# Performance work log

Measured on AMD Instinct MI355X. Metric: run time of the kernel, lower is better.

## Reference

```python
import jax, jax.numpy as jnp
import numpy as np

HIDDEN = 768
META = 25
ED_COUNT = 300
B, N_MENT, N_PAIRS = 2, 2000, 40000


def setup_inputs() -> dict:
    key = jax.random.key(0)
    ks = jax.random.split(key, 8)
    mention_reprs = jax.random.normal(ks[0], (B, N_MENT, HIDDEN), dtype=jnp.float32)
    coref_mention_pairs = jax.random.randint(ks[1], (B, N_PAIRS, 2), 0, N_MENT)
    coref_eds = jax.random.randint(ks[2], (B, N_PAIRS), 0, ED_COUNT)
    in_dim = HIDDEN * 2 + META
    # nn.Linear default init scale ~ 1/sqrt(fan_in); exact init is irrelevant for correctness
    W1 = jax.random.normal(ks[3], (in_dim, HIDDEN), dtype=jnp.float32) / np.sqrt(in_dim)
    b1 = jnp.zeros((HIDDEN,), dtype=jnp.float32)
    W2 = jax.random.normal(ks[4], (HIDDEN, 1), dtype=jnp.float32) / np.sqrt(HIDDEN)
    b2 = jnp.zeros((1,), dtype=jnp.float32)
    ed_table = jax.random.normal(ks[5], (ED_COUNT, META), dtype=jnp.float32)
    return {
        "mention_reprs": mention_reprs,
        "coref_mention_pairs": coref_mention_pairs,
        "coref_eds": coref_eds,
        "ed_table": ed_table,
        "W1": W1,
        "b1": b1,
        "W2": W2,
        "b2": b2,
    }


def reference(mention_reprs, coref_mention_pairs, coref_eds, ed_table, W1, b1, W2, b2):
    b = mention_reprs.shape[0]
    # batch_index gather: [B, P, 2, H]
    bidx = jnp.arange(b)[:, None, None]
    pairs = mention_reprs[bidx, coref_mention_pairs]
    # flatten pair dim -> [B, P, 2H]
    pair_repr = pairs.reshape(b, pairs.shape[1], -1)
    eds = ed_table[coref_eds]  # [B, P, META]
    coref_repr = jnp.concatenate([pair_repr, eds], axis=2)  # [B, P, 2H+META]
    h = jax.nn.relu(coref_repr @ W1 + b1)  # dropout = identity in eval
    logits = (h @ W2 + b2).squeeze(-1)  # [B, P]
    return logits
```

## Files before the change

### kernel.cpp

```cpp
#include <hip/hip_runtime.h>
#include <stdint.h>

#define HIDDEN 768
#define META 25
#define EDC 300
#define BB 2
#define NMENT 2000
#define NPAIRS 40000
#define M_ROWS (BB * NMENT)
#define M_PAD 4096
#define N_OUT 1536
#define TOTAL_PAIRS (BB * NPAIRS)
#define BK 64

typedef __bf16 bf16x8 __attribute__((ext_vector_type(8)));
typedef float f32x4 __attribute__((ext_vector_type(4)));

static __device__ __forceinline__ float bf2f(unsigned short u) {
    union { unsigned int u; float f; } v; v.u = ((unsigned int)u) << 16; return v.f;
}
static __device__ __forceinline__ float2 bf2x(unsigned int u) {
    union { unsigned int x; float f; } lo, hi;
    lo.x = u << 16; hi.x = u & 0xffff0000u;
    float2 r; r.x = lo.f; r.y = hi.f; return r;
}
static __device__ __forceinline__ unsigned short f2bf(float f) {
    union { float f; unsigned int u; } v; v.f = f;
    unsigned int u = v.u;
    unsigned int r = (u + 0x7FFFu + ((u >> 16) & 1u)) >> 16;
    return (unsigned short)r;
}

#define GLOAD_LDS16(g, l)                                                            \
    __builtin_amdgcn_global_load_lds((const __attribute__((address_space(1))) void*)(g), \
                                     (__attribute__((address_space(3))) void*)(l), 16, 0, 0)

#define NB_CONVM 3072
#define NB_CONVW 576
#define NB_PREP  900
#define NB_W2    3

__global__ __launch_bounds__(256) void k_prep_all(
        const float* __restrict__ M, unsigned short* __restrict__ Mb,
        const float* __restrict__ W1, unsigned short* __restrict__ Wt,
        const float* __restrict__ ed_table, const float* __restrict__ b1,
        unsigned short* __restrict__ Epp,
        const float* __restrict__ W2, unsigned short* __restrict__ W2b) {
    const int blk = blockIdx.x;
    const int t = threadIdx.x;
    if (blk < NB_CONVM) {
        int idx = (blk * 256 + t) * 4;
        int row = idx / HIDDEN;
        ushort4 o;
        if (row < M_ROWS) {
            const float4 v = *(const float4*)(M + idx);
            o.x = f2bf(v.x); o.y = f2bf(v.y); o.z = f2bf(v.z); o.w = f2bf(v.w);
        } else {
            o.x = 0; o.y = 0; o.z = 0; o.w = 0;
        }
        *(ushort4*)(Mb + idx) = o;
    } else if (blk < NB_CONVM + NB_CONVW) {
        __shared__ float tile[32][68];
        int id = blk - NB_CONVM;
        int nt = id % 24, kt = id / 24;
        int n0 = nt * 64, k0 = kt * 32;
        int tk = t >> 4, tn = (t & 15) * 4;
        int srcRowOff = (n0 < HIDDEN) ? 0 : HIDDEN;
        int srcColBase = (n0 < HIDDEN) ? n0 : (n0 - HIDDEN);
        {
            const float4 v0 = *(const float4*)(W1 + (size_t)(k0 + tk + srcRowOff) * HIDDEN + srcColBase + tn);
            tile[tk][tn] = v0.x; tile[tk][tn + 1] = v0.y; tile[tk][tn + 2] = v0.z; tile[tk][tn + 3] = v0.w;
            const float4 v1 = *(const float4*)(W1 + (size_t)(k0 + tk + 16 + srcRowOff) * HIDDEN + srcColBase + tn);
            tile[tk + 16][tn] = v1.x; tile[tk + 16][tn + 1] = v1.y; tile[tk + 16][tn + 2] = v1.z; tile[tk + 16][tn + 3] = v1.w;
        }
        __syncthreads();
        int wn = t >> 2, wk = (t & 3) * 8;
        unsigned int p0 = (unsigned int)f2bf(tile[wk + 0][wn]) | ((unsigned int)f2bf(tile[wk + 1][wn]) << 16);
        unsigned int p1 = (unsigned int)f2bf(tile[wk + 2][wn]) | ((unsigned int)f2bf(tile[wk + 3][wn]) << 16);
        unsigned int p2 = (unsigned int)f2bf(tile[wk + 4][wn]) | ((unsigned int)f2bf(tile[wk + 5][wn]) << 16);
        unsigned int p3 = (unsigned int)f2bf(tile[wk + 6][wn]) | ((unsigned int)f2bf(tile[wk + 7][wn]) << 16);
        uint4 pk; pk.x = p0; pk.y = p1; pk.z = p2; pk.w = p3;
        *(uint4*)(Wt + (size_t)(n0 + wn) * HIDDEN + k0 + wk) = pk;
    } else if (blk < NB_CONVM + NB_CONVW + NB_PREP) {
        int id = (blk - NB_CONVM - NB_CONVW) * 256 + t;
        int e = id / HIDDEN, n = id - e * HIDDEN;
        float acc = b1[n];
#pragma unroll
        for (int k = 0; k < META; k++)
            acc += ed_table[e * META + k] * W1[(size_t)(2 * HIDDEN + k) * HIDDEN + n];
        Epp[id] = f2bf(acc);
    } else {
        int id = (blk - NB_CONVM - NB_CONVW - NB_PREP) * 256 + t;
        if (id < HIDDEN) W2b[id] = f2bf(W2[id]);
    }
}

__global__ __launch_bounds__(256) void k_gemm(const unsigned short* __restrict__ Mb,
                                              const unsigned short* __restrict__ Wt,
                                              unsigned short* __restrict__ AW) {
    __shared__ unsigned short As[128 * BK];
    __shared__ unsigned short Bs[64 * BK];
    const int m0 = blockIdx.x * 128;
    const int n0 = blockIdx.y * 64;
    const int t = threadIdx.x, w = t >> 6, lane = t & 63;
    const int wm = (w & 1) * 64, wn = (w >> 1) * 32;
    const int q = lane >> 4, r = lane & 15;
    const int lrow = lane >> 3;
    const int lcol = ((((lane & 7) - lrow) & 7)) * 8;
    const unsigned short* gA = Mb + (size_t)(m0 + w * 32 + lrow) * HIDDEN + lcol;
    const unsigned short* gB = Wt + (size_t)(n0 + w * 16 + lrow) * HIDDEN + lcol;
    unsigned short* lA = As + (w * 32) * BK;
    unsigned short* lB = Bs + (w * 16) * BK;
    f32x4 acc[4][2] = {};
    for (int k0 = 0; k0 < HIDDEN; k0 += BK) {
        GLOAD_LDS16(gA + k0, lA);
        GLOAD_LDS16(gA + k0 + 8 * HIDDEN,  lA + 8 * BK);
        GLOAD_LDS16(gA + k0 + 16 * HIDDEN, lA + 16 * BK);
        GLOAD_LDS16(gA + k0 + 24 * HIDDEN, lA + 24 * BK);
        GLOAD_LDS16(gB + k0, lB);
        GLOAD_LDS16(gB + k0 + 8 * HIDDEN,  lB + 8 * BK);
        __syncthreads();
        bf16x8 af[4][2], bfr[2][2];
        const int rs = r & 7;
#pragma unroll
        for (int i = 0; i < 4; i++)
#pragma unroll
            for (int s = 0; s < 2; s++)
                af[i][s] = *(const bf16x8*)&As[(wm + i * 16 + r) * BK + 8 * ((q + 4 * s + rs) & 7)];
#pragma unroll
        for (int j = 0; j < 2; j++)
#pragma unroll
            for (int s = 0; s < 2; s++)
                bfr[j][s] = *(const bf16x8*)&Bs[(wn + j * 16 + r) * BK + 8 * ((q + 4 * s + rs) & 7)];
#pragma unroll
        for (int i = 0; i < 4; i++)
#pragma unroll
            for (int j = 0; j < 2; j++) {
                acc[i][j] = __builtin_amdgcn_mfma_f32_16x16x32_bf16(af[i][0], bfr[j][0], acc[i][j], 0, 0, 0);
                acc[i][j] = __builtin_amdgcn_mfma_f32_16x16x32_bf16(af[i][1], bfr[j][1], acc[i][j], 0, 0, 0);
            }
        __syncthreads();
    }
    const int colb = n0 + wn + (lane & 15);
    const int rowb = m0 + wm + (lane >> 4) * 4;
#pragma unroll
    for (int i = 0; i < 4; i++)
#pragma unroll
        for (int j = 0; j < 2; j++) {
            unsigned short* dst = AW + (size_t)(rowb + i * 16) * N_OUT + colb + j * 16;
#pragma unroll
            for (int reg = 0; reg < 4; reg++)
                dst[(size_t)reg * N_OUT] = f2bf(acc[i][j][reg]);
        }
}

__global__ __launch_bounds__(256) void k_pair(const unsigned short* __restrict__ AW,
                                              const unsigned short* __restrict__ Epp,
                                              const unsigned short* __restrict__ W2b,
                                              const float* __restrict__ b2,
                                              const int* __restrict__ pairs,
                                              const int* __restrict__ eds,
                                              float* __restrict__ out) {
    const int wid = blockIdx.x * 4 + (threadIdx.x >> 6);
    const int lane = threadIdx.x & 63;
    const int p0 = wid * 4;
    const int b = (p0 >= NPAIRS) ? 1 : 0;
    const int n0 = lane * 8;
    const int n1 = 512 + (lane & 31) * 8;
    const bool lo = lane < 32;

    const int4 pr01 = *(const int4*)(pairs + (size_t)p0 * 2);
    const int4 pr23 = *(const int4*)(pairs + (size_t)p0 * 2 + 4);
    const int4 ed4  = *(const int4*)(eds + p0);

    const size_t base = (size_t)(b * NMENT);
    const unsigned short* a1p0 = AW + (base + pr01.x) * N_OUT;
    const unsigned short* a2p0 = AW + (base + pr01.y) * N_OUT + HIDDEN;
    const unsigned short* ep0  = Epp + (size_t)ed4.x * HIDDEN;
    const unsigned short* a1p1 = AW + (base + pr01.z) * N_OUT;
    const unsigned short* a2p1 = AW + (base + pr01.w) * N_OUT + HIDDEN;
    const unsigned short* ep1  = Epp + (size_t)ed4.y * HIDDEN;
    const unsigned short* a1p2 = AW + (base + pr23.x) * N_OUT;
    const unsigned short* a2p2 = AW + (base + pr23.y) * N_OUT + HIDDEN;
    const unsigned short* ep2  = Epp + (size_t)ed4.z * HIDDEN;
    const unsigned short* a1p3 = AW + (base + pr23.z) * N_OUT;
    const unsigned short* a2p3 = AW + (base + pr23.w) * N_OUT + HIDDEN;
    const unsigned short* ep3  = Epp + (size_t)ed4.w * HIDDEN;

    const unsigned short* c01a = lo ? a1p0 : a1p1;
    const unsigned short* c01b = lo ? a2p0 : a2p1;
    const unsigned short* c01e = lo ? ep0  : ep1;
    const unsigned short* c23a = lo ? a1p2 : a1p3;
    const unsigned short* c23b = lo ? a2p2 : a2p3;
    const unsigned short* c23e = lo ? ep2  : ep3;

    uint4 w0 = *(const uint4*)(W2b + n0);
    uint4 wc = *(const uint4*)(W2b + n1);
    uint4 x1 = *(const uint4*)(a1p0 + n0), x2 = *(const uint4*)(a2p0 + n0), xe = *(const uint4*)(ep0 + n0);
    uint4 y1 = *(const uint4*)(a1p1 + n0), y2 = *(const uint4*)(a2p1 + n0), ye = *(const uint4*)(ep1 + n0);
    uint4 z1 = *(const uint4*)(a1p2 + n0), z2 = *(const uint4*)(a2p2 + n0), ze = *(const uint4*)(ep2 + n0);
    uint4 v1 = *(const uint4*)(a1p3 + n0), v2 = *(const uint4*)(a2p3 + n0), ve = *(const uint4*)(ep3 + n0);
    uint4 q1 = *(const uint4*)(c01a + n1), q2 = *(const uint4*)(c01b + n1), qe = *(const uint4*)(c01e + n1);
    uint4 s1 = *(const uint4*)(c23a + n1), s2 = *(const uint4*)(c23b + n1), se = *(const uint4*)(c23e + n1);

    float acc0 = 0.f, acc1 = 0.f, acc2 = 0.f, acc3 = 0.f;
    float cacc01 = 0.f, cacc23 = 0.f;
#define ACC2(acc, ua, ub, ue, uw)                                              \
    {                                                                          \
        float2 fa = bf2x(ua), fb = bf2x(ub), fe = bf2x(ue), fw = bf2x(uw);     \
        float h0 = fmaxf(fa.x + fb.x + fe.x, 0.f);                             \
        float h1 = fmaxf(fa.y + fb.y + fe.y, 0.f);                             \
        acc += h0 * fw.x + h1 * fw.y;                                          \
    }
    ACC2(acc0, x1.x, x2.x, xe.x, w0.x); ACC2(acc0, x1.y, x2.y, xe.y, w0.y);
    ACC2(acc0, x1.z, x2.z, xe.z, w0.z); ACC2(acc0, x1.w, x2.w, xe.w, w0.w);
    ACC2(acc1, y1.x, y2.x, ye.x, w0.x); ACC2(acc1, y1.y, y2.y, ye.y, w0.y);
    ACC2(acc1, y1.z, y2.z, ye.z, w0.z); ACC2(acc1, y1.w, y2.w, ye.w, w0.w);
    ACC2(acc2, z1.x, z2.x, ze.x, w0.x); ACC2(acc2, z1.y, z2.y, ze.y, w0.y);
    ACC2(acc2, z1.z, z2.z, ze.z, w0.z); ACC2(acc2, z1.w, z2.w, ze.w, w0.w);
    ACC2(acc3, v1.x, v2.x, ve.x, w0.x); ACC2(acc3, v1.y, v2.y, ve.y, w0.y);
    ACC2(acc3, v1.z, v2.z, ve.z, w0.z); ACC2(acc3, v1.w, v2.w, ve.w, w0.w);
    ACC2(cacc01, q1.x, q2.x, qe.x, wc.x); ACC2(cacc01, q1.y, q2.y, qe.y, wc.y);
    ACC2(cacc01, q1.z, q2.z, qe.z, wc.z); ACC2(cacc01, q1.w, q2.w, qe.w, wc.w);
    ACC2(cacc23, s1.x, s2.x, se.x, wc.x); ACC2(cacc23, s1.y, s2.y, se.y, wc.y);
    ACC2(cacc23, s1.z, s2.z, se.z, wc.z); ACC2(cacc23, s1.w, s2.w, se.w, wc.w);
#undef ACC2
#pragma unroll
    for (int o = 32; o > 0; o >>= 1) {
        acc0 += __shfl_xor(acc0, o, 64);
        acc1 += __shfl_xor(acc1, o, 64);
        acc2 += __shfl_xor(acc2, o, 64);
        acc3 += __shfl_xor(acc3, o, 64);
    }
#pragma unroll
    for (int o = 16; o > 0; o >>= 1) {
        cacc01 += __shfl_xor(cacc01, o, 64);
        cacc23 += __shfl_xor(cacc23, o, 64);
    }
    const float t0 = __shfl(cacc01, 0, 64);
    const float t1 = __shfl(cacc01, 32, 64);
    const float t2 = __shfl(cacc23, 0, 64);
    const float t3 = __shfl(cacc23, 32, 64);
    if (lane == 0) {
        float bias = b2[0];
        float4 o;
        o.x = acc0 + t0 + bias;
        o.y = acc1 + t1 + bias;
        o.z = acc2 + t2 + bias;
        o.w = acc3 + t3 + bias;
        *(float4*)(out + p0) = o;
    }
}

extern "C" void kernel_launch(void* const* d_in, const int* in_sizes, int n_in,
                              void* d_out, int out_size, void* d_ws, size_t ws_size,
                              hipStream_t stream) {
    const float* mention  = (const float*)d_in[0];
    const int*   pairs    = (const int*)d_in[1];
    const int*   eds      = (const int*)d_in[2];
    const float* ed_table = (const float*)d_in[3];
    const float* W1       = (const float*)d_in[4];
    const float* b1       = (const float*)d_in[5];
    const float* W2       = (const float*)d_in[6];
    const float* b2       = (const float*)d_in[7];
    float* out = (float*)d_out;

    char* ws = (char*)d_ws;
    unsigned short* Mb  = (unsigned short*)(ws);
    unsigned short* Wt  = (unsigned short*)(ws + 6291456);
    unsigned short* AW  = (unsigned short*)(ws + 8650752);
    unsigned short* Epp = (unsigned short*)(ws + 21233664);
    unsigned short* W2b = (unsigned short*)(ws + 21694464);

    k_prep_all<<<dim3(NB_CONVM + NB_CONVW + NB_PREP + NB_W2), dim3(256), 0, stream>>>(
        mention, Mb, W1, Wt, ed_table, b1, Epp, W2, W2b);
    k_gemm<<<dim3(M_PAD / 128, N_OUT / 64), dim3(256), 0, stream>>>(Mb, Wt, AW);
    k_pair<<<dim3(TOTAL_PAIRS / 16), dim3(256), 0, stream>>>(AW, Epp, W2b, b2, pairs, eds, out);
}
```

Measured before the change: 115.8 us.

## Fuse prep, GEMM and pair kernels into one cooperative persistent kernel

Merges the three launches (conversion/prep, bf16 GEMM, pair gather-reduce) into a single cooperative kernel. Blocks loop over the former grid indices, and grid-wide syncs separate the phases. The aim is to remove launch overhead and inter-kernel gaps. In exchange it adds grid barrier costs and caps the grid at resident occupancy (at most 768 blocks), which can reduce latency hiding in the memory-bound pair phase.

```diff
diff --git a/kernel.cpp b/kernel.cpp
--- a/kernel.cpp
+++ b/kernel.cpp
@@ -1,5 +1,8 @@
 #include <hip/hip_runtime.h>
+#include <hip/hip_cooperative_groups.h>
 #include <stdint.h>
+
+namespace cg = cooperative_groups;
 
 #define HIDDEN 768
 #define META 25
@@ -16,9 +19,6 @@
 typedef __bf16 bf16x8 __attribute__((ext_vector_type(8)));
 typedef float f32x4 __attribute__((ext_vector_type(4)));
 
-static __device__ __forceinline__ float bf2f(unsigned short u) {
-    union { unsigned int u; float f; } v; v.u = ((unsigned int)u) << 16; return v.f;
-}
 static __device__ __forceinline__ float2 bf2x(unsigned int u) {
     union { unsigned int x; float f; } lo, hi;
     lo.x = u << 16; hi.x = u & 0xffff0000u;
@@ -39,172 +39,180 @@
 #define NB_CONVW 576
 #define NB_PREP  900
 #define NB_W2    3
-
-__global__ __launch_bounds__(256) void k_prep_all(
+#define NB_TOT   (NB_CONVM + NB_CONVW + NB_PREP + NB_W2)
+#define NB_GEMM  768
+#define NB_PAIR  (TOTAL_PAIRS / 16)
+
+__global__ __launch_bounds__(256, 3) void k_fused(
         const float* __restrict__ M, unsigned short* __restrict__ Mb,
         const float* __restrict__ W1, unsigned short* __restrict__ Wt,
         const float* __restrict__ ed_table, const float* __restrict__ b1,
         unsigned short* __restrict__ Epp,
-        const float* __restrict__ W2, unsigned short* __restrict__ W2b) {
-    const int blk = blockIdx.x;
-    const int t = threadIdx.x;
-    if (blk < NB_CONVM) {
-        int idx = (blk * 256 + t) * 4;
-        int row = idx / HIDDEN;
-        ushort4 o;
-        if (row < M_ROWS) {
-            const float4 v = *(const float4*)(M + idx);
-            o.x = f2bf(v.x); o.y = f2bf(v.y); o.z = f2bf(v.z); o.w = f2bf(v.w);
-        } else {
-            o.x = 0; o.y = 0; o.z = 0; o.w = 0;
-        }
-        *(ushort4*)(Mb + idx) = o;
-    } else if (blk < NB_CONVM + NB_CONVW) {
-        __shared__ float tile[32][68];
-        int id = blk - NB_CONVM;
-        int nt = id % 24, kt = id / 24;
-        int n0 = nt * 64, k0 = kt * 32;
-        int tk = t >> 4, tn = (t & 15) * 4;
-        int srcRowOff = (n0 < HIDDEN) ? 0 : HIDDEN;
-        int srcColBase = (n0 < HIDDEN) ? n0 : (n0 - HIDDEN);
-        {
-            const float4 v0 = *(const float4*)(W1 + (size_t)(k0 + tk + srcRowOff) * HIDDEN + srcColBase + tn);
-            tile[tk][tn] = v0.x; tile[tk][tn + 1] = v0.y; tile[tk][tn + 2] = v0.z; tile[tk][tn + 3] = v0.w;
-            const float4 v1 = *(const float4*)(W1 + (size_t)(k0 + tk + 16 + srcRowOff) * HIDDEN + srcColBase + tn);
-            tile[tk + 16][tn] = v1.x; tile[tk + 16][tn + 1] = v1.y; tile[tk + 16][tn + 2] = v1.z; tile[tk + 16][tn + 3] = v1.w;
-        }
-        __syncthreads();
-        int wn = t >> 2, wk = (t & 3) * 8;
-        unsigned int p0 = (unsigned int)f2bf(tile[wk + 0][wn]) | ((unsigned int)f2bf(tile[wk + 1][wn]) << 16);
-        unsigned int p1 = (unsigned int)f2bf(tile[wk + 2][wn]) | ((unsigned int)f2bf(tile[wk + 3][wn]) << 16);
-        unsigned int p2 = (unsigned int)f2bf(tile[wk + 4][wn]) | ((unsigned int)f2bf(tile[wk + 5][wn]) << 16);
-        unsigned int p3 = (unsigned int)f2bf(tile[wk + 6][wn]) | ((unsigned int)f2bf(tile[wk + 7][wn]) << 16);
-        uint4 pk; pk.x = p0; pk.y = p1; pk.z = p2; pk.w = p3;
-        *(uint4*)(Wt + (size_t)(n0 + wn) * HIDDEN + k0 + wk) = pk;
-    } else if (blk < NB_CONVM + NB_CONVW + NB_PREP) {
-        int id = (blk - NB_CONVM - NB_CONVW) * 256 + t;
-        int e = id / HIDDEN, n = id - e * HIDDEN;
-        float acc = b1[n];
-#pragma unroll
-        for (int k = 0; k < META; k++)
-            acc += ed_table[e * META + k] * W1[(size_t)(2 * HIDDEN + k) * HIDDEN + n];
-        Epp[id] = f2bf(acc);
-    } else {
-        int id = (blk - NB_CONVM - NB_CONVW - NB_PREP) * 256 + t;
-        if (id < HIDDEN) W2b[id] = f2bf(W2[id]);
-    }
-}
-
-__global__ __launch_bounds__(256) void k_gemm(const unsigned short* __restrict__ Mb,
-                                              const unsigned short* __restrict__ Wt,
-                                              unsigned short* __restrict__ AW) {
+        const float* __restrict__ W2, unsigned short* __restrict__ W2b,
+        const float* __restrict__ b2,
+        const int* __restrict__ pairs, const int* __restrict__ eds,
+        unsigned short* __restrict__ AW, float* __restrict__ out) {
     __shared__ unsigned short As[128 * BK];
     __shared__ unsigned short Bs[64 * BK];
-    const int m0 = blockIdx.x * 128;
-    const int n0 = blockIdx.y * 64;
-    const int t = threadIdx.x, w = t >> 6, lane = t & 63;
-    const int wm = (w & 1) * 64, wn = (w >> 1) * 32;
-    const int q = lane >> 4, r = lane & 15;
-    const int lrow = lane >> 3;
-    const int lcol = ((((lane & 7) - lrow) & 7)) * 8;
-    const unsigned short* gA = Mb + (size_t)(m0 + w * 32 + lrow) * HIDDEN + lcol;
-    const unsigned short* gB = Wt + (size_t)(n0 + w * 16 + lrow) * HIDDEN + lcol;
-    unsigned short* lA = As + (w * 32) * BK;
-    unsigned short* lB = Bs + (w * 16) * BK;
-    f32x4 acc[4][2] = {};
-    for (int k0 = 0; k0 < HIDDEN; k0 += BK) {
-        GLOAD_LDS16(gA + k0, lA);
-        GLOAD_LDS16(gA + k0 + 8 * HIDDEN,  lA + 8 * BK);
-        GLOAD_LDS16(gA + k0 + 16 * HIDDEN, lA + 16 * BK);
-        GLOAD_LDS16(gA + k0 + 24 * HIDDEN, lA + 24 * BK);
-        GLOAD_LDS16(gB + k0, lB);
-        GLOAD_LDS16(gB + k0 + 8 * HIDDEN,  lB + 8 * BK);
-        __syncthreads();
-        bf16x8 af[4][2], bfr[2][2];
-        const int rs = r & 7;
-#pragma unroll
-        for (int i = 0; i < 4; i++)
-#pragma unroll
-            for (int s = 0; s < 2; s++)
-                af[i][s] = *(const bf16x8*)&As[(wm + i * 16 + r) * BK + 8 * ((q + 4 * s + rs) & 7)];
-#pragma unroll
-        for (int j = 0; j < 2; j++)
-#pragma unroll
-            for (int s = 0; s < 2; s++)
-                bfr[j][s] = *(const bf16x8*)&Bs[(wn + j * 16 + r) * BK + 8 * ((q + 4 * s + rs) & 7)];
-#pragma unroll
-        for (int i = 0; i < 4; i++)
-#pragma unroll
-            for (int j = 0; j < 2; j++) {
-                acc[i][j] = __builtin_amdgcn_mfma_f32_16x16x32_bf16(af[i][0], bfr[j][0], acc[i][j], 0, 0, 0);
-                acc[i][j] = __builtin_amdgcn_mfma_f32_16x16x32_bf16(af[i][1], bfr[j][1], acc[i][j], 0, 0, 0);
-            }
-        __syncthreads();
-    }
-    const int colb = n0 + wn + (lane & 15);
-    const int rowb = m0 + wm + (lane >> 4) * 4;
-#pragma unroll
-    for (int i = 0; i < 4; i++)
-#pragma unroll
-        for (int j = 0; j < 2; j++) {
-            unsigned short* dst = AW + (size_t)(rowb + i * 16) * N_OUT + colb + j * 16;
-#pragma unroll
-            for (int reg = 0; reg < 4; reg++)
-                dst[(size_t)reg * N_OUT] = f2bf(acc[i][j][reg]);
+    __shared__ float tile[32][68];
+    const int t = threadIdx.x;
+    const int NG = gridDim.x;
+
+    for (int blk = blockIdx.x; blk < NB_TOT; blk += NG) {
+        if (blk < NB_CONVM) {
+            int idx = (blk * 256 + t) * 4;
+            int row = idx / HIDDEN;
+            ushort4 o;
+            if (row < M_ROWS) {
+                const float4 v = *(const float4*)(M + idx);
+                o.x = f2bf(v.x); o.y = f2bf(v.y); o.z = f2bf(v.z); o.w = f2bf(v.w);
+            } else {
+                o.x = 0; o.y = 0; o.z = 0; o.w = 0;
+            }
+            *(ushort4*)(Mb + idx) = o;
+        } else if (blk < NB_CONVM + NB_CONVW) {
+            int id = blk - NB_CONVM;
+            int nt = id % 24, kt = id / 24;
+            int n0 = nt * 64, k0 = kt * 32;
+            int tk = t >> 4, tn = (t & 15) * 4;
+            int srcRowOff = (n0 < HIDDEN) ? 0 : HIDDEN;
+            int srcColBase = (n0 < HIDDEN) ? n0 : (n0 - HIDDEN);
+            {
+                const float4 v0 = *(const float4*)(W1 + (size_t)(k0 + tk + srcRowOff) * HIDDEN + srcColBase + tn);
+                tile[tk][tn] = v0.x; tile[tk][tn + 1] = v0.y; tile[tk][tn + 2] = v0.z; tile[tk][tn + 3] = v0.w;
+                const float4 v1 = *(const float4*)(W1 + (size_t)(k0 + tk + 16 + srcRowOff) * HIDDEN + srcColBase + tn);
+                tile[tk + 16][tn] = v1.x; tile[tk + 16][tn + 1] = v1.y; tile[tk + 16][tn + 2] = v1.z; tile[tk + 16][tn + 3] = v1.w;
+            }
+            __syncthreads();
+            int wn = t >> 2, wk = (t & 3) * 8;
+            unsigned int p0 = (unsigned int)f2bf(tile[wk + 0][wn]) | ((unsigned int)f2bf(tile[wk + 1][wn]) << 16);
+            unsigned int p1 = (unsigned int)f2bf(tile[wk + 2][wn]) | ((unsigned int)f2bf(tile[wk + 3][wn]) << 16);
+            unsigned int p2 = (unsigned int)f2bf(tile[wk + 4][wn]) | ((unsigned int)f2bf(tile[wk + 5][wn]) << 16);
+            unsigned int p3 = (unsigned int)f2bf(tile[wk + 6][wn]) | ((unsigned int)f2bf(tile[wk + 7][wn]) << 16);
+            uint4 pk; pk.x = p0; pk.y = p1; pk.z = p2; pk.w = p3;
+            *(uint4*)(Wt + (size_t)(n0 + wn) * HIDDEN + k0 + wk) = pk;
+            __syncthreads();
+        } else if (blk < NB_CONVM + NB_CONVW + NB_PREP) {
+            int id = (blk - NB_CONVM - NB_CONVW) * 256 + t;
+            int e = id / HIDDEN, n = id - e * HIDDEN;
+            float acc = b1[n];
+#pragma unroll
+            for (int k = 0; k < META; k++)
+                acc += ed_table[e * META + k] * W1[(size_t)(2 * HIDDEN + k) * HIDDEN + n];
+            Epp[id] = f2bf(acc);
+        } else {
+            int id = (blk - NB_CONVM - NB_CONVW - NB_PREP) * 256 + t;
+            if (id < HIDDEN) W2b[id] = f2bf(W2[id]);
         }
-}
-
-__global__ __launch_bounds__(256) void k_pair(const unsigned short* __restrict__ AW,
-                                              const unsigned short* __restrict__ Epp,
-                                              const unsigned short* __restrict__ W2b,
-                                              const float* __restrict__ b2,
-                                              const int* __restrict__ pairs,
-                                              const int* __restrict__ eds,
-                                              float* __restrict__ out) {
-    const int wid = blockIdx.x * 4 + (threadIdx.x >> 6);
-    const int lane = threadIdx.x & 63;
-    const int p0 = wid * 4;
-    const int b = (p0 >= NPAIRS) ? 1 : 0;
-    const int n0 = lane * 8;
-    const int n1 = 512 + (lane & 31) * 8;
-    const bool lo = lane < 32;
-
-    const int4 pr01 = *(const int4*)(pairs + (size_t)p0 * 2);
-    const int4 pr23 = *(const int4*)(pairs + (size_t)p0 * 2 + 4);
-    const int4 ed4  = *(const int4*)(eds + p0);
-
-    const size_t base = (size_t)(b * NMENT);
-    const unsigned short* a1p0 = AW + (base + pr01.x) * N_OUT;
-    const unsigned short* a2p0 = AW + (base + pr01.y) * N_OUT + HIDDEN;
-    const unsigned short* ep0  = Epp + (size_t)ed4.x * HIDDEN;
-    const unsigned short* a1p1 = AW + (base + pr01.z) * N_OUT;
-    const unsigned short* a2p1 = AW + (base + pr01.w) * N_OUT + HIDDEN;
-    const unsigned short* ep1  = Epp + (size_t)ed4.y * HIDDEN;
-    const unsigned short* a1p2 = AW + (base + pr23.x) * N_OUT;
-    const unsigned short* a2p2 = AW + (base + pr23.y) * N_OUT + HIDDEN;
-    const unsigned short* ep2  = Epp + (size_t)ed4.z * HIDDEN;
-    const unsigned short* a1p3 = AW + (base + pr23.z) * N_OUT;
-    const unsigned short* a2p3 = AW + (base + pr23.w) * N_OUT + HIDDEN;
-    const unsigned short* ep3  = Epp + (size_t)ed4.w * HIDDEN;
-
-    const unsigned short* c01a = lo ? a1p0 : a1p1;
-    const unsigned short* c01b = lo ? a2p0 : a2p1;
-    const unsigned short* c01e = lo ? ep0  : ep1;
-    const unsigned short* c23a = lo ? a1p2 : a1p3;
-    const unsigned short* c23b = lo ? a2p2 : a2p3;
-    const unsigned short* c23e = lo ? ep2  : ep3;
-
-    uint4 w0 = *(const uint4*)(W2b + n0);
-    uint4 wc = *(const uint4*)(W2b + n1);
-    uint4 x1 = *(const uint4*)(a1p0 + n0), x2 = *(const uint4*)(a2p0 + n0), xe = *(const uint4*)(ep0 + n0);
-    uint4 y1 = *(const uint4*)(a1p1 + n0), y2 = *(const uint4*)(a2p1 + n0), ye = *(const uint4*)(ep1 + n0);
-    uint4 z1 = *(const uint4*)(a1p2 + n0), z2 = *(const uint4*)(a2p2 + n0), ze = *(const uint4*)(ep2 + n0);
-    uint4 v1 = *(const uint4*)(a1p3 + n0), v2 = *(const uint4*)(a2p3 + n0), ve = *(const uint4*)(ep3 + n0);
-    uint4 q1 = *(const uint4*)(c01a + n1), q2 = *(const uint4*)(c01b + n1), qe = *(const uint4*)(c01e + n1);
-    uint4 s1 = *(const uint4*)(c23a + n1), s2 = *(const uint4*)(c23b + n1), se = *(const uint4*)(c23e + n1);
-
-    float acc0 = 0.f, acc1 = 0.f, acc2 = 0.f, acc3 = 0.f;
-    float cacc01 = 0.f, cacc23 = 0.f;
+    }
+    __threadfence();
+    cg::this_grid().sync();
+
+    {
+        const int w = t >> 6, lane = t & 63;
+        const int wm = (w & 1) * 64, wn = (w >> 1) * 32;
+        const int q = lane >> 4, r = lane & 15;
+        const int lrow = lane >> 3;
+        const int lcol = ((((lane & 7) - lrow) & 7)) * 8;
+        unsigned short* lA = As + (w * 32) * BK;
+        unsigned short* lB = Bs + (w * 16) * BK;
+        for (int v = blockIdx.x; v < NB_GEMM; v += NG) {
+            const int m0 = (v & 31) * 128;
+            const int n0 = (v >> 5) * 64;
+            const unsigned short* gA = Mb + (size_t)(m0 + w * 32 + lrow) * HIDDEN + lcol;
+            const unsigned short* gB = Wt + (size_t)(n0 + w * 16 + lrow) * HIDDEN + lcol;
+            f32x4 acc[4][2] = {};
+            for (int k0 = 0; k0 < HIDDEN; k0 += BK) {
+                GLOAD_LDS16(gA + k0, lA);
+                GLOAD_LDS16(gA + k0 + 8 * HIDDEN,  lA + 8 * BK);
+                GLOAD_LDS16(gA + k0 + 16 * HIDDEN, lA + 16 * BK);
+                GLOAD_LDS16(gA + k0 + 24 * HIDDEN, lA + 24 * BK);
+                GLOAD_LDS16(gB + k0, lB);
+                GLOAD_LDS16(gB + k0 + 8 * HIDDEN,  lB + 8 * BK);
+                __syncthreads();
+                bf16x8 af[4][2], bfr[2][2];
+                const int rs = r & 7;
+#pragma unroll
+                for (int i = 0; i < 4; i++)
+#pragma unroll
+                    for (int s = 0; s < 2; s++)
+                        af[i][s] = *(const bf16x8*)&As[(wm + i * 16 + r) * BK + 8 * ((q + 4 * s + rs) & 7)];
+#pragma unroll
+                for (int j = 0; j < 2; j++)
+#pragma unroll
+                    for (int s = 0; s < 2; s++)
+                        bfr[j][s] = *(const bf16x8*)&Bs[(wn + j * 16 + r) * BK + 8 * ((q + 4 * s + rs) & 7)];
+#pragma unroll
+                for (int i = 0; i < 4; i++)
+#pragma unroll
+                    for (int j = 0; j < 2; j++) {
+                        acc[i][j] = __builtin_amdgcn_mfma_f32_16x16x32_bf16(af[i][0], bfr[j][0], acc[i][j], 0, 0, 0);
+                        acc[i][j] = __builtin_amdgcn_mfma_f32_16x16x32_bf16(af[i][1], bfr[j][1], acc[i][j], 0, 0, 0);
+                    }
+                __syncthreads();
+            }
+            const int colb = n0 + wn + (lane & 15);
+            const int rowb = m0 + wm + (lane >> 4) * 4;
+#pragma unroll
+            for (int i = 0; i < 4; i++)
+#pragma unroll
+                for (int j = 0; j < 2; j++) {
+                    unsigned short* dst = AW + (size_t)(rowb + i * 16) * N_OUT + colb + j * 16;
+#pragma unroll
+                    for (int reg = 0; reg < 4; reg++)
+                        dst[(size_t)reg * N_OUT] = f2bf(acc[i][j][reg]);
+                }
+        }
+    }
+    __threadfence();
+    cg::this_grid().sync();
+
+    {
+        const int lane = t & 63;
+        const int n0 = lane * 8;
+        const int n1 = 512 + (lane & 31) * 8;
+        const bool lo = lane < 32;
+        for (int v = blockIdx.x; v < NB_PAIR; v += NG) {
+            const int wid = v * 4 + (t >> 6);
+            const int p0 = wid * 4;
+            const int b = (p0 >= NPAIRS) ? 1 : 0;
+
+            const int4 pr01 = *(const int4*)(pairs + (size_t)p0 * 2);
+            const int4 pr23 = *(const int4*)(pairs + (size_t)p0 * 2 + 4);
+            const int4 ed4  = *(const int4*)(eds + p0);
+
+            const size_t base = (size_t)(b * NMENT);
+            const unsigned short* a1p0 = AW + (base + pr01.x) * N_OUT;
+            const unsigned short* a2p0 = AW + (base + pr01.y) * N_OUT + HIDDEN;
+            const unsigned short* ep0  = Epp + (size_t)ed4.x * HIDDEN;
+            const unsigned short* a1p1 = AW + (base + pr01.z) * N_OUT;
+            const unsigned short* a2p1 = AW + (base + pr01.w) * N_OUT + HIDDEN;
+            const unsigned short* ep1  = Epp + (size_t)ed4.y * HIDDEN;
+            const unsigned short* a1p2 = AW + (base + pr23.x) * N_OUT;
+            const unsigned short* a2p2 = AW + (base + pr23.y) * N_OUT + HIDDEN;
+            const unsigned short* ep2  = Epp + (size_t)ed4.z * HIDDEN;
+            const unsigned short* a1p3 = AW + (base + pr23.z) * N_OUT;
+            const unsigned short* a2p3 = AW + (base + pr23.w) * N_OUT + HIDDEN;
+            const unsigned short* ep3  = Epp + (size_t)ed4.w * HIDDEN;
+
+            const unsigned short* c01a = lo ? a1p0 : a1p1;
+            const unsigned short* c01b = lo ? a2p0 : a2p1;
+            const unsigned short* c01e = lo ? ep0  : ep1;
+            const unsigned short* c23a = lo ? a1p2 : a1p3;
+            const unsigned short* c23b = lo ? a2p2 : a2p3;
+            const unsigned short* c23e = lo ? ep2  : ep3;
+
+            uint4 w0 = *(const uint4*)(W2b + n0);
+            uint4 wc = *(const uint4*)(W2b + n1);
+            uint4 x1 = *(const uint4*)(a1p0 + n0), x2 = *(const uint4*)(a2p0 + n0), xe = *(const uint4*)(ep0 + n0);
+            uint4 y1 = *(const uint4*)(a1p1 + n0), y2 = *(const uint4*)(a2p1 + n0), ye = *(const uint4*)(ep1 + n0);
+            uint4 z1 = *(const uint4*)(a1p2 + n0), z2 = *(const uint4*)(a2p2 + n0), ze = *(const uint4*)(ep2 + n0);
+            uint4 v1 = *(const uint4*)(a1p3 + n0), v2 = *(const uint4*)(a2p3 + n0), ve = *(const uint4*)(ep3 + n0);
+            uint4 q1 = *(const uint4*)(c01a + n1), q2 = *(const uint4*)(c01b + n1), qe = *(const uint4*)(c01e + n1);
+            uint4 s1 = *(const uint4*)(c23a + n1), s2 = *(const uint4*)(c23b + n1), se = *(const uint4*)(c23e + n1);
+
+            float acc0 = 0.f, acc1 = 0.f, acc2 = 0.f, acc3 = 0.f;
+            float cacc01 = 0.f, cacc23 = 0.f;
 #define ACC2(acc, ua, ub, ue, uw)                                              \
     {                                                                          \
         float2 fa = bf2x(ua), fb = bf2x(ub), fe = bf2x(ue), fw = bf2x(uw);     \
@@ -212,43 +220,45 @@
         float h1 = fmaxf(fa.y + fb.y + fe.y, 0.f);                             \
         acc += h0 * fw.x + h1 * fw.y;                                          \
     }
-    ACC2(acc0, x1.x, x2.x, xe.x, w0.x); ACC2(acc0, x1.y, x2.y, xe.y, w0.y);
-    ACC2(acc0, x1.z, x2.z, xe.z, w0.z); ACC2(acc0, x1.w, x2.w, xe.w, w0.w);
-    ACC2(acc1, y1.x, y2.x, ye.x, w0.x); ACC2(acc1, y1.y, y2.y, ye.y, w0.y);
-    ACC2(acc1, y1.z, y2.z, ye.z, w0.z); ACC2(acc1, y1.w, y2.w, ye.w, w0.w);
-    ACC2(acc2, z1.x, z2.x, ze.x, w0.x); ACC2(acc2, z1.y, z2.y, ze.y, w0.y);
-    ACC2(acc2, z1.z, z2.z, ze.z, w0.z); ACC2(acc2, z1.w, z2.w, ze.w, w0.w);
-    ACC2(acc3, v1.x, v2.x, ve.x, w0.x); ACC2(acc3, v1.y, v2.y, ve.y, w0.y);
-    ACC2(acc3, v1.z, v2.z, ve.z, w0.z); ACC2(acc3, v1.w, v2.w, ve.w, w0.w);
-    ACC2(cacc01, q1.x, q2.x, qe.x, wc.x); ACC2(cacc01, q1.y, q2.y, qe.y, wc.y);
-    ACC2(cacc01, q1.z, q2.z, qe.z, wc.z); ACC2(cacc01, q1.w, q2.w, qe.w, wc.w);
-    ACC2(cacc23, s1.x, s2.x, se.x, wc.x); ACC2(cacc23, s1.y, s2.y, se.y, wc.y);
-    ACC2(cacc23, s1.z, s2.z, se.z, wc.z); ACC2(cacc23, s1.w, s2.w, se.w, wc.w);
+            ACC2(acc0, x1.x, x2.x, xe.x, w0.x); ACC2(acc0, x1.y, x2.y, xe.y, w0.y);
+            ACC2(acc0, x1.z, x2.z, xe.z, w0.z); ACC2(acc0, x1.w, x2.w, xe.w, w0.w);
+            ACC2(acc1, y1.x, y2.x, ye.x, w0.x); ACC2(acc1, y1.y, y2.y, ye.y, w0.y);
+            ACC2(acc1, y1.z, y2.z, ye.z, w0.z); ACC2(acc1, y1.w, y2.w, ye.w, w0.w);
+            ACC2(acc2, z1.x, z2.x, ze.x, w0.x); ACC2(acc2, z1.y, z2.y, ze.y, w0.y);
+            ACC2(acc2, z1.z, z2.z, ze.z, w0.z); ACC2(acc2, z1.w, z2.w, ze.w, w0.w);
+            ACC2(acc3, v1.x, v2.x, ve.x, w0.x); ACC2(acc3, v1.y, v2.y, ve.y, w0.y);
+            ACC2(acc3, v1.z, v2.z, ve.z, w0.z); ACC2(acc3, v1.w, v2.w, ve.w, w0.w);
+            ACC2(cacc01, q1.x, q2.x, qe.x, wc.x); ACC2(cacc01, q1.y, q2.y, qe.y, wc.y);
+            ACC2(cacc01, q1.z, q2.z, qe.z, wc.z); ACC2(cacc01, q1.w, q2.w, qe.w, wc.w);
+            ACC2(cacc23, s1.x, s2.x, se.x, wc.x); ACC2(cacc23, s1.y, s2.y, se.y, wc.y);
+            ACC2(cacc23, s1.z, s2.z, se.z, wc.z); ACC2(cacc23, s1.w, s2.w, se.w, wc.w);
 #undef ACC2
 #pragma unroll
-    for (int o = 32; o > 0; o >>= 1) {
-        acc0 += __shfl_xor(acc0, o, 64);
-        acc1 += __shfl_xor(acc1, o, 64);
-        acc2 += __shfl_xor(acc2, o, 64);
-        acc3 += __shfl_xor(acc3, o, 64);
-    }
-#pragma unroll
-    for (int o = 16; o > 0; o >>= 1) {
-        cacc01 += __shfl_xor(cacc01, o, 64);
-        cacc23 += __shfl_xor(cacc23, o, 64);
-    }
-    const float t0 = __shfl(cacc01, 0, 64);
-    const float t1 = __shfl(cacc01, 32, 64);
-    const float t2 = __shfl(cacc23, 0, 64);
-    const float t3 = __shfl(cacc23, 32, 64);
-    if (lane == 0) {
-        float bias = b2[0];
-        float4 o;
-        o.x = acc0 + t0 + bias;
-        o.y = acc1 + t1 + bias;
-        o.z = acc2 + t2 + bias;
-        o.w = acc3 + t3 + bias;
-        *(float4*)(out + p0) = o;
+            for (int o = 32; o > 0; o >>= 1) {
+                acc0 += __shfl_xor(acc0, o, 64);
+                acc1 += __shfl_xor(acc1, o, 64);
+                acc2 += __shfl_xor(acc2, o, 64);
+                acc3 += __shfl_xor(acc3, o, 64);
+            }
+#pragma unroll
+            for (int o = 16; o > 0; o >>= 1) {
+                cacc01 += __shfl_xor(cacc01, o, 64);
+                cacc23 += __shfl_xor(cacc23, o, 64);
+            }
+            const float t0 = __shfl(cacc01, 0, 64);
+            const float t1 = __shfl(cacc01, 32, 64);
+            const float t2 = __shfl(cacc23, 0, 64);
+            const float t3 = __shfl(cacc23, 32, 64);
+            if (lane == 0) {
+                float bias = b2[0];
+                float4 o;
+                o.x = acc0 + t0 + bias;
+                o.y = acc1 + t1 + bias;
+                o.z = acc2 + t2 + bias;
+                o.w = acc3 + t3 + bias;
+                *(float4*)(out + p0) = o;
+            }
+        }
     }
 }
 
@@ -272,8 +282,20 @@
     unsigned short* Epp = (unsigned short*)(ws + 21233664);
     unsigned short* W2b = (unsigned short*)(ws + 21694464);
 
-    k_prep_all<<<dim3(NB_CONVM + NB_CONVW + NB_PREP + NB_W2), dim3(256), 0, stream>>>(
-        mention, Mb, W1, Wt, ed_table, b1, Epp, W2, W2b);
-    k_gemm<<<dim3(M_PAD / 128, N_OUT / 64), dim3(256), 0, stream>>>(Mb, Wt, AW);
-    k_pair<<<dim3(TOTAL_PAIRS / 16), dim3(256), 0, stream>>>(AW, Epp, W2b, b2, pairs, eds, out);
+    static int gridSize = 0;
+    if (gridSize == 0) {
+        int nb = 0;
+        hipOccupancyMaxActiveBlocksPerMultiprocessor(&nb, k_fused, 256, 0);
+        if (nb < 1) nb = 1;
+        long g = (long)nb * 256;
+        gridSize = (int)(g < NB_GEMM ? g : NB_GEMM);
+    }
+    void* args[] = {
+        (void*)&mention, (void*)&Mb, (void*)&W1, (void*)&Wt,
+        (void*)&ed_table, (void*)&b1, (void*)&Epp,
+        (void*)&W2, (void*)&W2b, (void*)&b2,
+        (void*)&pairs, (void*)&eds, (void*)&AW, (void*)&out
+    };
+    hipLaunchCooperativeKernel(reinterpret_cast<void*>(k_fused),
+                               dim3(gridSize), dim3(256), args, 0, stream);
 }
```

Result: slower. 363.8 us (+214.2%).
